# Kernel tuning notes

Hardware: AMD Instinct MI355X
Metric: run time of the kernel (lower is better)

## Reference

```python
import jax, jax.numpy as jnp
import numpy as np
import math

NUM_CLASSES = 80
IOU_LOSS_THRESH = 0.5
ANCHORS = [
    np.array([[12, 16], [19, 36], [40, 28]], dtype=np.float32),
    np.array([[36, 75], [76, 55], [72, 146]], dtype=np.float32),
    np.array([[142, 110], [192, 243], [459, 401]], dtype=np.float32),
]


def decode(conv, anchors, stride, num_class):
    B, S = conv.shape[0], conv.shape[1]
    A = anchors.shape[0]
    conv = conv.reshape(B, S, S, A, 5 + num_class)
    dxdy = conv[..., 0:2]
    dwdh = conv[..., 2:4]
    dconf = conv[..., 4:5]
    dprob = conv[..., 5:]
    r = jnp.arange(S, dtype=conv.dtype)
    # matches torch: offset[..., 0] varies along dim2, offset[..., 1] along dim1
    offset = jnp.stack([jnp.broadcast_to(r[None, :], (S, S)),
                        jnp.broadcast_to(r[:, None], (S, S))], axis=-1)
    offset = offset[None, :, :, None, :]  # (1,S,S,1,2)
    pred_xy = (jax.nn.sigmoid(dxdy) + offset) * stride
    pred_wh = jnp.exp(dwdh) * jnp.asarray(anchors)  # (A,2) broadcast
    return jnp.concatenate([pred_xy, pred_wh,
                            jax.nn.sigmoid(dconf), jax.nn.sigmoid(dprob)], axis=-1)


def _to_corners(b):
    return jnp.concatenate([b[..., :2] - b[..., 2:] * 0.5,
                            b[..., :2] + b[..., 2:] * 0.5], axis=-1)


def bbox_ciou(boxes1, boxes2):
    b1 = _to_corners(boxes1)
    b2 = _to_corners(boxes2)
    b1 = jnp.concatenate([jnp.minimum(b1[..., :2], b1[..., 2:]),
                          jnp.maximum(b1[..., :2], b1[..., 2:])], axis=-1)
    b2 = jnp.concatenate([jnp.minimum(b2[..., :2], b2[..., 2:]),
                          jnp.maximum(b2[..., :2], b2[..., 2:])], axis=-1)
    area1 = (b1[..., 2] - b1[..., 0]) * (b1[..., 3] - b1[..., 1])
    area2 = (b2[..., 2] - b2[..., 0]) * (b2[..., 3] - b2[..., 1])
    lu = jnp.maximum(b1[..., :2], b2[..., :2])
    rd = jnp.minimum(b1[..., 2:], b2[..., 2:])
    inter = jnp.maximum(rd - lu, 0.0)
    inter_area = inter[..., 0] * inter[..., 1]
    union = area1 + area2 - inter_area
    iou = inter_area / (union + 1e-9)
    enc_lu = jnp.minimum(b1[..., :2], b2[..., :2])
    enc_rd = jnp.maximum(b1[..., 2:], b2[..., 2:])
    enc_wh = enc_rd - enc_lu
    c2 = enc_wh[..., 0] ** 2 + enc_wh[..., 1] ** 2
    p2 = (boxes1[..., 0] - boxes2[..., 0]) ** 2 + (boxes1[..., 1] - boxes2[..., 1]) ** 2
    atan1 = jnp.arctan(boxes1[..., 2] / (boxes1[..., 3] + 1e-9))
    atan2 = jnp.arctan(boxes2[..., 2] / (boxes2[..., 3] + 1e-9))
    v = 4.0 * (atan1 - atan2) ** 2 / (math.pi ** 2)
    a = v / (1.0 - iou + v)
    return iou - p2 / c2 - a * v


def bbox_iou(boxes1, boxes2):
    area1 = boxes1[..., 2] * boxes1[..., 3]
    area2 = boxes2[..., 2] * boxes2[..., 3]
    b1 = _to_corners(boxes1)
    b2 = _to_corners(boxes2)
    lu = jnp.maximum(b1[..., :2], b2[..., :2])
    rd = jnp.minimum(b1[..., 2:], b2[..., 2:])
    inter = jnp.maximum(rd - lu, 0.0)
    inter_area = inter[..., 0] * inter[..., 1]
    union = area1 + area2 - inter_area
    return inter_area / union


def loss_layer(conv, pred, label, bboxes, stride, num_class, iou_loss_thresh):
    B, S = conv.shape[0], conv.shape[1]
    input_size = float(stride * S)
    pred_xywh = pred[..., 0:4]
    pred_conf = pred[..., 4:5]
    pred_prob = pred[..., 5:]
    label_xywh = label[..., 0:4]
    respond_bbox = label[..., 4:5]
    label_prob = label[..., 5:]

    ciou = bbox_ciou(pred_xywh, label_xywh)[..., None]  # (B,S,S,3,1)
    bbox_loss_scale = 2.0 - label_xywh[..., 2:3] * label_xywh[..., 3:4] / input_size ** 2
    ciou_loss = respond_bbox * bbox_loss_scale * (1.0 - ciou)

    prob_pos = label_prob * (-jnp.log(pred_prob + 1e-9))
    prob_neg = (1.0 - label_prob) * (-jnp.log(1.0 - pred_prob + 1e-9))
    prob_loss = respond_bbox * (prob_pos + prob_neg)

    iou = bbox_iou(pred_xywh[:, :, :, :, None, :],
                   bboxes[:, None, None, None, :, :])  # (B,S,S,3,70)
    max_iou = jnp.max(iou, axis=-1, keepdims=True)
    respond_bgd = (1.0 - respond_bbox) * (max_iou < iou_loss_thresh).astype(pred.dtype)
    pos_loss = respond_bbox * (-jnp.log(pred_conf + 1e-9))
    neg_loss = respond_bgd * (-jnp.log(1.0 - pred_conf + 1e-9))
    conf_loss = pos_loss + neg_loss

    ciou_loss = ciou_loss.sum(axis=(1, 2, 3, 4)).mean()
    conf_loss = conf_loss.sum(axis=(1, 2, 3, 4)).mean()
    prob_loss = prob_loss.sum(axis=(1, 2, 3, 4)).mean()
    return ciou_loss, conf_loss, prob_loss


def setup_inputs() -> dict:
    key = jax.random.key(0)
    ks = jax.random.split(key, 7)
    B, NC = 16, NUM_CLASSES
    C = 3 * (5 + NC)
    inp = {
        'conv_lbbox': jax.random.normal(ks[0], (B, 19, 19, C), jnp.float32),
        'conv_mbbox': jax.random.normal(ks[1], (B, 38, 38, C), jnp.float32),
        'conv_sbbox': jax.random.normal(ks[2], (B, 76, 76, C), jnp.float32),
        'label_sbbox': jax.random.uniform(ks[3], (B, 76, 76, 3, 5 + NC), jnp.float32),
        'label_mbbox': jax.random.uniform(ks[4], (B, 38, 38, 3, 5 + NC), jnp.float32),
        'label_lbbox': jax.random.uniform(ks[5], (B, 19, 19, 3, 5 + NC), jnp.float32),
        'true_bboxes': jax.random.uniform(ks[6], (B, 70, 4), jnp.float32, 1.0, 600.0),
    }
    return inp


def reference(conv_lbbox, conv_mbbox, conv_sbbox, label_sbbox, label_mbbox,
              label_lbbox, true_bboxes):
    nc, thr = NUM_CLASSES, IOU_LOSS_THRESH
    pred_s = decode(conv_sbbox, ANCHORS[0], 8, nc)
    pred_m = decode(conv_mbbox, ANCHORS[1], 16, nc)
    pred_l = decode(conv_lbbox, ANCHORS[2], 32, nc)
    s_ciou, s_conf, s_prob = loss_layer(conv_sbbox, pred_s, label_sbbox, true_bboxes, 8, nc, thr)
    m_ciou, m_conf, m_prob = loss_layer(conv_mbbox, pred_m, label_mbbox, true_bboxes, 16, nc, thr)
    l_ciou, l_conf, l_prob = loss_layer(conv_lbbox, pred_l, label_lbbox, true_bboxes, 32, nc, thr)
    ciou_loss = s_ciou + m_ciou + l_ciou
    conf_loss = s_conf + m_conf + l_conf
    prob_loss = s_prob + m_prob + l_prob
    all_loss = ciou_loss + conf_loss + prob_loss
    return (all_loss, ciou_loss, conf_loss, prob_loss)
```

## Files before the change

kernel.cpp:

```cpp
#include <hip/hip_runtime.h>
#include <math.h>

#define NCLS 80
#define CH 85

static constexpr int RS = 16 * 76 * 76 * 3;
static constexpr int RM = 16 * 38 * 38 * 3;
static constexpr int RL = 16 * 19 * 19 * 3;

static constexpr int BS_BLK = RS / 256;
static constexpr int BM_BLK = (RM + 255) / 256;
static constexpr int BL_BLK = (RL + 255) / 256;
static constexpr int NBLK   = BS_BLK + BM_BLK + BL_BLK;

__constant__ float c_anchors[18] = {
    12.f, 16.f, 19.f, 36.f, 40.f, 28.f,
    36.f, 75.f, 76.f, 55.f, 72.f, 146.f,
    142.f, 110.f, 192.f, 243.f, 459.f, 401.f
};

__device__ __forceinline__ float fast_rcp(float x) {
    return __builtin_amdgcn_rcpf(x);
}
__device__ __forceinline__ float sigm(float x) {
    return fast_rcp(1.f + __expf(-x));
}
__device__ __forceinline__ float softplusf(float x) {
    return fmaxf(x, 0.f) + __logf(1.f + __expf(-fabsf(x)));
}

__global__ __launch_bounds__(256) void yolo_main(
    const float* __restrict__ conv_l, const float* __restrict__ conv_m,
    const float* __restrict__ conv_s, const float* __restrict__ lab_s,
    const float* __restrict__ lab_m, const float* __restrict__ lab_l,
    const float* __restrict__ tb, float* __restrict__ pb)
{
    int blk = blockIdx.x;

    const float* conv; const float* lab;
    int S; float stride; int ao; int blkLocal; int nrec_scale;
    if (blk < BS_BLK) {
        conv = conv_s; lab = lab_s; S = 76; stride = 8.f;  ao = 0;
        blkLocal = blk;                 nrec_scale = RS;
    } else if (blk < BS_BLK + BM_BLK) {
        conv = conv_m; lab = lab_m; S = 38; stride = 16.f; ao = 6;
        blkLocal = blk - BS_BLK;        nrec_scale = RM;
    } else {
        conv = conv_l; lab = lab_l; S = 19; stride = 32.f; ao = 12;
        blkLocal = blk - BS_BLK - BM_BLK; nrec_scale = RL;
    }

    int r0   = blkLocal * 256;
    int nrec = min(256, nrec_scale - r0);
    int E    = nrec * 85;
    int n4   = E >> 2;

    const float* cbase = conv + (size_t)r0 * CH;
    const float* lbase = lab  + (size_t)r0 * CH;

    __shared__ float convA[256 * 5];
    __shared__ float labA[256 * 5];

    float ciou_acc = 0.f, conf_acc = 0.f, prob_acc = 0.f;

    for (int i4 = threadIdx.x; i4 < n4; i4 += 256) {
        int e = i4 << 2;
        float4 cv = *reinterpret_cast<const float4*>(cbase + e);
        float4 lv = *reinterpret_cast<const float4*>(lbase + e);
        float cvv[4] = {cv.x, cv.y, cv.z, cv.w};
        float lvv[4] = {lv.x, lv.y, lv.z, lv.w};

        unsigned rA  = (unsigned)e / 85u;
        unsigned bnd = (rA + 1u) * 85u;
        float respA = lbase[rA * 85u + 4u];
        unsigned rB = ((unsigned)(e + 3) >= bnd) ? rA + 1u : rA;
        float respB = lbase[rB * 85u + 4u];

        #pragma unroll
        for (int d = 0; d < 4; d++) {
            unsigned el = (unsigned)(e + d);
            bool nxt   = el >= bnd;
            unsigned r = nxt ? rA + 1u : rA;
            unsigned c = el - r * 85u;
            float x = cvv[d], l = lvv[d];
            if (c >= 5u) {
                float sp = softplusf(x);
                float resp = nxt ? respB : respA;
                prob_acc += resp * (sp - l * x);
            } else {
                convA[r * 5u + c] = x;
                labA[r * 5u + c]  = l;
            }
        }
    }
    __syncthreads();

    int t = threadIdx.x;
    if (t < nrec) {
        unsigned rl = (unsigned)(r0 + t);
        unsigned a = rl % 3u; unsigned q = rl / 3u;
        unsigned j = q % (unsigned)S; q /= (unsigned)S;
        unsigned i = q % (unsigned)S; unsigned b = q / (unsigned)S;

        float c0 = convA[t * 5 + 0], c1 = convA[t * 5 + 1], c2v = convA[t * 5 + 2];
        float c3 = convA[t * 5 + 3], c4 = convA[t * 5 + 4];
        float lx = labA[t * 5 + 0], ly = labA[t * 5 + 1], lw = labA[t * 5 + 2];
        float lh = labA[t * 5 + 3], resp = labA[t * 5 + 4];

        float px = (sigm(c0) + (float)j) * stride;
        float py = (sigm(c1) + (float)i) * stride;
        float pw = __expf(c2v) * c_anchors[ao + 2 * a];
        float ph = __expf(c3)  * c_anchors[ao + 2 * a + 1];

        float hx = 0.5f * pw, hy = 0.5f * ph;
        float b1x1 = px - hx, b1y1 = py - hy, b1x2 = px + hx, b1y2 = py + hy;
        float hlx = 0.5f * lw, hly = 0.5f * lh;
        float b2x1 = lx - hlx, b2y1 = ly - hly, b2x2 = lx + hlx, b2y2 = ly + hly;

        float area1 = (b1x2 - b1x1) * (b1y2 - b1y1);
        float area2 = (b2x2 - b2x1) * (b2y2 - b2y1);
        float lux = fmaxf(b1x1, b2x1), luy = fmaxf(b1y1, b2y1);
        float rdx = fminf(b1x2, b2x2), rdy = fminf(b1y2, b2y2);
        float iw = fmaxf(rdx - lux, 0.f), ih = fmaxf(rdy - luy, 0.f);
        float inter = iw * ih;
        float uni = area1 + area2 - inter;
        float iou = inter / (uni + 1e-9f);

        float encw = fmaxf(b1x2, b2x2) - fminf(b1x1, b2x1);
        float ench = fmaxf(b1y2, b2y2) - fminf(b1y1, b2y1);
        float cc2 = encw * encw + ench * ench;
        float dx = px - lx, dy = py - ly;
        float p2 = dx * dx + dy * dy;
        float at1 = atanf(pw / (ph + 1e-9f));
        float at2 = atanf(lw / (lh + 1e-9f));
        float dat = at1 - at2;
        const float FOUR_OVER_PI2 = 0.40528473456935109f;
        float v = FOUR_OVER_PI2 * dat * dat;
        float al = v / (1.f - iou + v);
        float ciou = iou - p2 / cc2 - al * v;
        float bscale = 2.f - lw * lh * (1.f / (608.f * 608.f));
        ciou_acc = resp * bscale * (1.f - ciou);

        const float* tbp = tb + (size_t)b * 70 * 4;
        float parea = pw * ph;
        float maxiou = 0.f;
        for (int n = 0; n < 70; n++) {
            float tx = tbp[4 * n], ty = tbp[4 * n + 1];
            float tw = tbp[4 * n + 2], th = tbp[4 * n + 3];
            float tx1 = tx - 0.5f * tw, ty1 = ty - 0.5f * th;
            float tx2 = tx + 0.5f * tw, ty2 = ty + 0.5f * th;
            float ix1 = fmaxf(b1x1, tx1), iy1 = fmaxf(b1y1, ty1);
            float ix2 = fminf(b1x2, tx2), iy2 = fminf(b1y2, ty2);
            float iiw = fmaxf(ix2 - ix1, 0.f), iih = fmaxf(iy2 - iy1, 0.f);
            float ia = iiw * iih;
            float u = parea + tw * th - ia;
            maxiou = fmaxf(maxiou, ia * fast_rcp(u));
        }
        float rbgd = (1.f - resp) * (maxiou < 0.5f ? 1.f : 0.f);
        float spc = softplusf(c4);
        conf_acc = resp * (spc - c4) + rbgd * spc;
    }

    for (int off = 32; off > 0; off >>= 1) {
        ciou_acc += __shfl_down(ciou_acc, off);
        conf_acc += __shfl_down(conf_acc, off);
        prob_acc += __shfl_down(prob_acc, off);
    }
    __shared__ float red[4][3];
    int lane = threadIdx.x & 63, wv = threadIdx.x >> 6;
    if (lane == 0) { red[wv][0] = ciou_acc; red[wv][1] = conf_acc; red[wv][2] = prob_acc; }
    __syncthreads();
    if (threadIdx.x == 0) {
        pb[blk]            = red[0][0] + red[1][0] + red[2][0] + red[3][0];
        pb[NBLK + blk]     = red[0][1] + red[1][1] + red[2][1] + red[3][1];
        pb[2 * NBLK + blk] = red[0][2] + red[1][2] + red[2][2] + red[3][2];
    }
}

__global__ __launch_bounds__(256) void finalize_k(const float* __restrict__ pb,
                                                  float* __restrict__ out)
{
    double s0 = 0.0, s1 = 0.0, s2 = 0.0;
    for (int i = threadIdx.x; i < NBLK; i += 256) {
        s0 += (double)pb[i];
        s1 += (double)pb[NBLK + i];
        s2 += (double)pb[2 * NBLK + i];
    }
    for (int off = 32; off > 0; off >>= 1) {
        s0 += __shfl_down(s0, off);
        s1 += __shfl_down(s1, off);
        s2 += __shfl_down(s2, off);
    }
    __shared__ double rd[4][3];
    int lane = threadIdx.x & 63, wv = threadIdx.x >> 6;
    if (lane == 0) { rd[wv][0] = s0; rd[wv][1] = s1; rd[wv][2] = s2; }
    __syncthreads();
    if (threadIdx.x == 0) {
        float ci = (float)((rd[0][0] + rd[1][0] + rd[2][0] + rd[3][0]) / 16.0);
        float co = (float)((rd[0][1] + rd[1][1] + rd[2][1] + rd[3][1]) / 16.0);
        float pr = (float)((rd[0][2] + rd[1][2] + rd[2][2] + rd[3][2]) / 16.0);
        out[0] = ci + co + pr;
        out[1] = ci;
        out[2] = co;
        out[3] = pr;
    }
}

extern "C" void kernel_launch(void* const* d_in, const int* in_sizes, int n_in,
                              void* d_out, int out_size, void* d_ws, size_t ws_size,
                              hipStream_t stream) {
    const float* conv_l = (const float*)d_in[0];
    const float* conv_m = (const float*)d_in[1];
    const float* conv_s = (const float*)d_in[2];
    const float* lab_s  = (const float*)d_in[3];
    const float* lab_m  = (const float*)d_in[4];
    const float* lab_l  = (const float*)d_in[5];
    const float* tb     = (const float*)d_in[6];
    float* pb  = (float*)d_ws;
    float* out = (float*)d_out;

    yolo_main<<<NBLK, 256, 0, stream>>>(conv_l, conv_m, conv_s,
                                        lab_s, lab_m, lab_l, tb, pb);
    finalize_k<<<1, 256, 0, stream>>>(pb, out);
}
```

Before: 277.9 us.

## Split class-prob streaming and per-record CIoU work into separate block types

The single fused block type is split in two. One set of blocks streams the full conv and label tensors in large coalesced float4 chunks, with 16 loads in flight per thread, and accumulates only the class-probability loss using a branchless mask. A second set of blocks handles one record per thread, reading the 5 box fields straight from global memory to compute CIoU, the max-IoU background mask and the confidence loss. This removes the shared-memory staging and the barrier between streaming and compute, and is meant to improve memory-level parallelism. In exchange, the first 5 channels of each record are read twice with strided uncoalesced loads.

```diff
diff --git a/kernel.cpp b/kernel.cpp
--- a/kernel.cpp
+++ b/kernel.cpp
@@ -1,17 +1,27 @@
 #include <hip/hip_runtime.h>
 #include <math.h>
 
-#define NCLS 80
 #define CH 85
 
 static constexpr int RS = 16 * 76 * 76 * 3;
 static constexpr int RM = 16 * 38 * 38 * 3;
 static constexpr int RL = 16 * 19 * 19 * 3;
 
-static constexpr int BS_BLK = RS / 256;
-static constexpr int BM_BLK = (RM + 255) / 256;
-static constexpr int BL_BLK = (RL + 255) / 256;
-static constexpr int NBLK   = BS_BLK + BM_BLK + BL_BLK;
+static constexpr int ES = RS * CH, EM = RM * CH, EL = RL * CH;
+static constexpr int FS = ES / 4, FM = EM / 4, FL = EL / 4;
+
+static constexpr int CHUNK = 4096;
+static constexpr int NBS = (FS + CHUNK - 1) / CHUNK;
+static constexpr int NBM = (FM + CHUNK - 1) / CHUNK;
+static constexpr int NBL = (FL + CHUNK - 1) / CHUNK;
+static constexpr int NBCE = NBS + NBM + NBL;
+
+static constexpr int QS = RS / 256;
+static constexpr int QM = (RM + 255) / 256;
+static constexpr int QL = (RL + 255) / 256;
+static constexpr int NQ = QS + QM + QL;
+
+static constexpr int NBLK = NBCE + NQ;
 
 __constant__ float c_anchors[18] = {
     12.f, 16.f, 19.f, 36.f, 40.f, 28.f,
@@ -19,12 +29,8 @@
     142.f, 110.f, 192.f, 243.f, 459.f, 401.f
 };
 
-__device__ __forceinline__ float fast_rcp(float x) {
-    return __builtin_amdgcn_rcpf(x);
-}
-__device__ __forceinline__ float sigm(float x) {
-    return fast_rcp(1.f + __expf(-x));
-}
+__device__ __forceinline__ float fast_rcp(float x) { return __builtin_amdgcn_rcpf(x); }
+__device__ __forceinline__ float sigm(float x)     { return fast_rcp(1.f + __expf(-x)); }
 __device__ __forceinline__ float softplusf(float x) {
     return fmaxf(x, 0.f) + __logf(1.f + __expf(-fabsf(x)));
 }
@@ -37,143 +43,151 @@
 {
     int blk = blockIdx.x;
 
-    const float* conv; const float* lab;
-    int S; float stride; int ao; int blkLocal; int nrec_scale;
-    if (blk < BS_BLK) {
-        conv = conv_s; lab = lab_s; S = 76; stride = 8.f;  ao = 0;
-        blkLocal = blk;                 nrec_scale = RS;
-    } else if (blk < BS_BLK + BM_BLK) {
-        conv = conv_m; lab = lab_m; S = 38; stride = 16.f; ao = 6;
-        blkLocal = blk - BS_BLK;        nrec_scale = RM;
+    if (blk < NBCE) {
+        const float* cbase; const float* lbase; int E; int q;
+        if (blk < NBS)            { q = blk;              cbase = conv_s; lbase = lab_s; E = ES; }
+        else if (blk < NBS + NBM) { q = blk - NBS;        cbase = conv_m; lbase = lab_m; E = EM; }
+        else                      { q = blk - NBS - NBM;  cbase = conv_l; lbase = lab_l; E = EL; }
+
+        int e = (q * CHUNK + (int)threadIdx.x) * 4;
+        unsigned r = (unsigned)e / 85u;
+        unsigned c = (unsigned)e - r * 85u;
+
+        float acc = 0.f;
+
+        #pragma unroll
+        for (int g = 0; g < 4; ++g) {
+            float4 cv[4], lv[4];
+            float  rsp[4];
+            unsigned cc[4];
+            int eloc = e; unsigned rr = r, ch = c;
+            #pragma unroll
+            for (int it = 0; it < 4; ++it) {
+                cc[it] = ch;
+                if (eloc < E) {
+                    cv[it]  = *reinterpret_cast<const float4*>(cbase + eloc);
+                    lv[it]  = *reinterpret_cast<const float4*>(lbase + eloc);
+                    rsp[it] = lbase[rr * 85u + 4u];
+                } else {
+                    cv[it] = make_float4(0.f, 0.f, 0.f, 0.f);
+                    lv[it] = make_float4(0.f, 0.f, 0.f, 0.f);
+                    rsp[it] = 0.f;
+                }
+                eloc += 1024; rr += 12u; ch += 4u;
+                if (ch >= 85u) { ch -= 85u; ++rr; }
+            }
+            e = eloc; r = rr; c = ch;
+
+            #pragma unroll
+            for (int it = 0; it < 4; ++it) {
+                float xs[4] = {cv[it].x, cv[it].y, cv[it].z, cv[it].w};
+                float ls[4] = {lv[it].x, lv[it].y, lv[it].z, lv[it].w};
+                #pragma unroll
+                for (int d = 0; d < 4; ++d) {
+                    unsigned cd = cc[it] + (unsigned)d;
+                    float w = (cd - 5u < 80u) ? rsp[it] : 0.f;
+                    float x = xs[d], l = ls[d];
+                    acc = fmaf(w, softplusf(x) - l * x, acc);
+                }
+            }
+        }
+
+        for (int off = 32; off > 0; off >>= 1) acc += __shfl_down(acc, off);
+        __shared__ float red[4];
+        int lane = threadIdx.x & 63, wv = threadIdx.x >> 6;
+        if (lane == 0) red[wv] = acc;
+        __syncthreads();
+        if (threadIdx.x == 0)
+            pb[2 * NQ + blk] = red[0] + red[1] + red[2] + red[3];
+
     } else {
-        conv = conv_l; lab = lab_l; S = 19; stride = 32.f; ao = 12;
-        blkLocal = blk - BS_BLK - BM_BLK; nrec_scale = RL;
-    }
-
-    int r0   = blkLocal * 256;
-    int nrec = min(256, nrec_scale - r0);
-    int E    = nrec * 85;
-    int n4   = E >> 2;
-
-    const float* cbase = conv + (size_t)r0 * CH;
-    const float* lbase = lab  + (size_t)r0 * CH;
-
-    __shared__ float convA[256 * 5];
-    __shared__ float labA[256 * 5];
-
-    float ciou_acc = 0.f, conf_acc = 0.f, prob_acc = 0.f;
-
-    for (int i4 = threadIdx.x; i4 < n4; i4 += 256) {
-        int e = i4 << 2;
-        float4 cv = *reinterpret_cast<const float4*>(cbase + e);
-        float4 lv = *reinterpret_cast<const float4*>(lbase + e);
-        float cvv[4] = {cv.x, cv.y, cv.z, cv.w};
-        float lvv[4] = {lv.x, lv.y, lv.z, lv.w};
-
-        unsigned rA  = (unsigned)e / 85u;
-        unsigned bnd = (rA + 1u) * 85u;
-        float respA = lbase[rA * 85u + 4u];
-        unsigned rB = ((unsigned)(e + 3) >= bnd) ? rA + 1u : rA;
-        float respB = lbase[rB * 85u + 4u];
-
-        #pragma unroll
-        for (int d = 0; d < 4; d++) {
-            unsigned el = (unsigned)(e + d);
-            bool nxt   = el >= bnd;
-            unsigned r = nxt ? rA + 1u : rA;
-            unsigned c = el - r * 85u;
-            float x = cvv[d], l = lvv[d];
-            if (c >= 5u) {
-                float sp = softplusf(x);
-                float resp = nxt ? respB : respA;
-                prob_acc += resp * (sp - l * x);
-            } else {
-                convA[r * 5u + c] = x;
-                labA[r * 5u + c]  = l;
+        int qb = blk - NBCE;
+        const float* conv; const float* lab;
+        int S; float stride; int ao; int r0; int nrec_scale;
+        if (qb < QS)           { conv = conv_s; lab = lab_s; S = 76; stride = 8.f;  ao = 0;  r0 = qb * 256;              nrec_scale = RS; }
+        else if (qb < QS + QM) { conv = conv_m; lab = lab_m; S = 38; stride = 16.f; ao = 6;  r0 = (qb - QS) * 256;       nrec_scale = RM; }
+        else                   { conv = conv_l; lab = lab_l; S = 19; stride = 32.f; ao = 12; r0 = (qb - QS - QM) * 256;  nrec_scale = RL; }
+
+        float ciou_acc = 0.f, conf_acc = 0.f;
+        int t = threadIdx.x;
+        int rec = r0 + t;
+        if (rec < nrec_scale) {
+            unsigned rl = (unsigned)rec;
+            unsigned a = rl % 3u; unsigned qq = rl / 3u;
+            unsigned j = qq % (unsigned)S; qq /= (unsigned)S;
+            unsigned i = qq % (unsigned)S; unsigned b = qq / (unsigned)S;
+
+            const float* cp = conv + (size_t)rec * CH;
+            const float* lp = lab  + (size_t)rec * CH;
+            float c0 = cp[0], c1 = cp[1], c2v = cp[2], c3 = cp[3], c4 = cp[4];
+            float lx = lp[0], ly = lp[1], lw = lp[2], lh = lp[3], resp = lp[4];
+
+            float px = (sigm(c0) + (float)j) * stride;
+            float py = (sigm(c1) + (float)i) * stride;
+            float pw = __expf(c2v) * c_anchors[ao + 2 * a];
+            float ph = __expf(c3)  * c_anchors[ao + 2 * a + 1];
+
+            float hx = 0.5f * pw, hy = 0.5f * ph;
+            float b1x1 = px - hx, b1y1 = py - hy, b1x2 = px + hx, b1y2 = py + hy;
+            float hlx = 0.5f * lw, hly = 0.5f * lh;
+            float b2x1 = lx - hlx, b2y1 = ly - hly, b2x2 = lx + hlx, b2y2 = ly + hly;
+
+            float area1 = (b1x2 - b1x1) * (b1y2 - b1y1);
+            float area2 = (b2x2 - b2x1) * (b2y2 - b2y1);
+            float lux = fmaxf(b1x1, b2x1), luy = fmaxf(b1y1, b2y1);
+            float rdx = fminf(b1x2, b2x2), rdy = fminf(b1y2, b2y2);
+            float iw = fmaxf(rdx - lux, 0.f), ih = fmaxf(rdy - luy, 0.f);
+            float inter = iw * ih;
+            float uni = area1 + area2 - inter;
+            float iou = inter / (uni + 1e-9f);
+
+            float encw = fmaxf(b1x2, b2x2) - fminf(b1x1, b2x1);
+            float ench = fmaxf(b1y2, b2y2) - fminf(b1y1, b2y1);
+            float cc2 = encw * encw + ench * ench;
+            float dx = px - lx, dy = py - ly;
+            float p2 = dx * dx + dy * dy;
+            float at1 = atanf(pw / (ph + 1e-9f));
+            float at2 = atanf(lw / (lh + 1e-9f));
+            float dat = at1 - at2;
+            const float FOUR_OVER_PI2 = 0.40528473456935109f;
+            float v = FOUR_OVER_PI2 * dat * dat;
+            float al = v / (1.f - iou + v);
+            float ciou = iou - p2 / cc2 - al * v;
+            float bscale = 2.f - lw * lh * (1.f / (608.f * 608.f));
+            ciou_acc = resp * bscale * (1.f - ciou);
+
+            const float* tbp = tb + (size_t)b * 70 * 4;
+            float parea = pw * ph;
+            float maxiou = 0.f;
+            for (int n = 0; n < 70; n++) {
+                float tx = tbp[4 * n], ty = tbp[4 * n + 1];
+                float tw = tbp[4 * n + 2], th = tbp[4 * n + 3];
+                float tx1 = tx - 0.5f * tw, ty1 = ty - 0.5f * th;
+                float tx2 = tx + 0.5f * tw, ty2 = ty + 0.5f * th;
+                float ix1 = fmaxf(b1x1, tx1), iy1 = fmaxf(b1y1, ty1);
+                float ix2 = fminf(b1x2, tx2), iy2 = fminf(b1y2, ty2);
+                float iiw = fmaxf(ix2 - ix1, 0.f), iih = fmaxf(iy2 - iy1, 0.f);
+                float ia = iiw * iih;
+                float u = parea + tw * th - ia;
+                maxiou = fmaxf(maxiou, ia * fast_rcp(u));
             }
-        }
-    }
-    __syncthreads();
-
-    int t = threadIdx.x;
-    if (t < nrec) {
-        unsigned rl = (unsigned)(r0 + t);
-        unsigned a = rl % 3u; unsigned q = rl / 3u;
-        unsigned j = q % (unsigned)S; q /= (unsigned)S;
-        unsigned i = q % (unsigned)S; unsigned b = q / (unsigned)S;
-
-        float c0 = convA[t * 5 + 0], c1 = convA[t * 5 + 1], c2v = convA[t * 5 + 2];
-        float c3 = convA[t * 5 + 3], c4 = convA[t * 5 + 4];
-        float lx = labA[t * 5 + 0], ly = labA[t * 5 + 1], lw = labA[t * 5 + 2];
-        float lh = labA[t * 5 + 3], resp = labA[t * 5 + 4];
-
-        float px = (sigm(c0) + (float)j) * stride;
-        float py = (sigm(c1) + (float)i) * stride;
-        float pw = __expf(c2v) * c_anchors[ao + 2 * a];
-        float ph = __expf(c3)  * c_anchors[ao + 2 * a + 1];
-
-        float hx = 0.5f * pw, hy = 0.5f * ph;
-        float b1x1 = px - hx, b1y1 = py - hy, b1x2 = px + hx, b1y2 = py + hy;
-        float hlx = 0.5f * lw, hly = 0.5f * lh;
-        float b2x1 = lx - hlx, b2y1 = ly - hly, b2x2 = lx + hlx, b2y2 = ly + hly;
-
-        float area1 = (b1x2 - b1x1) * (b1y2 - b1y1);
-        float area2 = (b2x2 - b2x1) * (b2y2 - b2y1);
-        float lux = fmaxf(b1x1, b2x1), luy = fmaxf(b1y1, b2y1);
-        float rdx = fminf(b1x2, b2x2), rdy = fminf(b1y2, b2y2);
-        float iw = fmaxf(rdx - lux, 0.f), ih = fmaxf(rdy - luy, 0.f);
-        float inter = iw * ih;
-        float uni = area1 + area2 - inter;
-        float iou = inter / (uni + 1e-9f);
-
-        float encw = fmaxf(b1x2, b2x2) - fminf(b1x1, b2x1);
-        float ench = fmaxf(b1y2, b2y2) - fminf(b1y1, b2y1);
-        float cc2 = encw * encw + ench * ench;
-        float dx = px - lx, dy = py - ly;
-        float p2 = dx * dx + dy * dy;
-        float at1 = atanf(pw / (ph + 1e-9f));
-        float at2 = atanf(lw / (lh + 1e-9f));
-        float dat = at1 - at2;
-        const float FOUR_OVER_PI2 = 0.40528473456935109f;
-        float v = FOUR_OVER_PI2 * dat * dat;
-        float al = v / (1.f - iou + v);
-        float ciou = iou - p2 / cc2 - al * v;
-        float bscale = 2.f - lw * lh * (1.f / (608.f * 608.f));
-        ciou_acc = resp * bscale * (1.f - ciou);
-
-        const float* tbp = tb + (size_t)b * 70 * 4;
-        float parea = pw * ph;
-        float maxiou = 0.f;
-        for (int n = 0; n < 70; n++) {
-            float tx = tbp[4 * n], ty = tbp[4 * n + 1];
-            float tw = tbp[4 * n + 2], th = tbp[4 * n + 3];
-            float tx1 = tx - 0.5f * tw, ty1 = ty - 0.5f * th;
-            float tx2 = tx + 0.5f * tw, ty2 = ty + 0.5f * th;
-            float ix1 = fmaxf(b1x1, tx1), iy1 = fmaxf(b1y1, ty1);
-            float ix2 = fminf(b1x2, tx2), iy2 = fminf(b1y2, ty2);
-            float iiw = fmaxf(ix2 - ix1, 0.f), iih = fmaxf(iy2 - iy1, 0.f);
-            float ia = iiw * iih;
-            float u = parea + tw * th - ia;
-            maxiou = fmaxf(maxiou, ia * fast_rcp(u));
-        }
-        float rbgd = (1.f - resp) * (maxiou < 0.5f ? 1.f : 0.f);
-        float spc = softplusf(c4);
-        conf_acc = resp * (spc - c4) + rbgd * spc;
-    }
-
-    for (int off = 32; off > 0; off >>= 1) {
-        ciou_acc += __shfl_down(ciou_acc, off);
-        conf_acc += __shfl_down(conf_acc, off);
-        prob_acc += __shfl_down(prob_acc, off);
-    }
-    __shared__ float red[4][3];
-    int lane = threadIdx.x & 63, wv = threadIdx.x >> 6;
-    if (lane == 0) { red[wv][0] = ciou_acc; red[wv][1] = conf_acc; red[wv][2] = prob_acc; }
-    __syncthreads();
-    if (threadIdx.x == 0) {
-        pb[blk]            = red[0][0] + red[1][0] + red[2][0] + red[3][0];
-        pb[NBLK + blk]     = red[0][1] + red[1][1] + red[2][1] + red[3][1];
-        pb[2 * NBLK + blk] = red[0][2] + red[1][2] + red[2][2] + red[3][2];
+            float rbgd = (1.f - resp) * (maxiou < 0.5f ? 1.f : 0.f);
+            float spc = softplusf(c4);
+            conf_acc = resp * (spc - c4) + rbgd * spc;
+        }
+
+        for (int off = 32; off > 0; off >>= 1) {
+            ciou_acc += __shfl_down(ciou_acc, off);
+            conf_acc += __shfl_down(conf_acc, off);
+        }
+        __shared__ float red2[4][2];
+        int lane = threadIdx.x & 63, wv = threadIdx.x >> 6;
+        if (lane == 0) { red2[wv][0] = ciou_acc; red2[wv][1] = conf_acc; }
+        __syncthreads();
+        if (threadIdx.x == 0) {
+            pb[qb]      = red2[0][0] + red2[1][0] + red2[2][0] + red2[3][0];
+            pb[NQ + qb] = red2[0][1] + red2[1][1] + red2[2][1] + red2[3][1];
+        }
     }
 }
 
@@ -181,10 +195,12 @@
                                                   float* __restrict__ out)
 {
     double s0 = 0.0, s1 = 0.0, s2 = 0.0;
-    for (int i = threadIdx.x; i < NBLK; i += 256) {
+    for (int i = threadIdx.x; i < NQ; i += 256) {
         s0 += (double)pb[i];
-        s1 += (double)pb[NBLK + i];
-        s2 += (double)pb[2 * NBLK + i];
+        s1 += (double)pb[NQ + i];
+    }
+    for (int i = threadIdx.x; i < NBCE; i += 256) {
+        s2 += (double)pb[2 * NQ + i];
     }
     for (int off = 32; off > 0; off >>= 1) {
         s0 += __shfl_down(s0, off);
```

Result: slower. 283.8 us (+2.1%).
